# Kernel optimization log

Hardware: AMD Instinct MI355X
Metric: run time of the kernel (lower is better)

Reference implementation:

```python
import jax, jax.numpy as jnp
import numpy as np

NEG_SLOPE = 0.2  # leakyrelu negative_slope from init

def _lrelu(x):
    return jax.nn.leaky_relu(x, NEG_SLOPE)

def setup_inputs() -> dict:
    key = jax.random.key(0)
    k1, k2, k3 = jax.random.split(key, 3)
    B, N, Fin, Fout = 8, 2048, 128, 64
    x = jax.random.normal(k1, (B, N, Fin), dtype=jnp.float32)
    W = jax.random.normal(k2, (Fin, Fout), dtype=jnp.float32) * (1.414 / np.sqrt(Fin))
    a = jax.random.normal(k3, (2 * Fout, 1), dtype=jnp.float32) * 0.1
    return {"x": x, "W": W, "a": a}

def reference(x, W, a):
    # x: (B, N, Fin), W: (Fin, Fout), a: (2*Fout, 1)
    Fout = W.shape[1]
    h = jnp.matmul(x, W)  # (B, N, Fout)
    a1 = a[:Fout, 0]      # attends to source node i
    a2 = a[Fout:, 0]      # attends to target node j
    # e[b,i,j] = leakyrelu(h[b,i]@a1 + h[b,j]@a2); avoids O(N^2*2F) repeat+cat
    s1 = jnp.einsum('bnf,f->bn', h, a1)  # (B, N)
    s2 = jnp.einsum('bnf,f->bn', h, a2)  # (B, N)
    e = _lrelu(s1[:, :, None] + s2[:, None, :])  # (B, N, N)
    attention = jax.nn.softmax(e, axis=1)  # softmax over dim=1, as in source
    # dropout in eval mode: identity
    h_prime = jnp.matmul(attention, h)  # (B, N, Fout)
    return _lrelu(h_prime)
```

## Files before the change

### kernel.cpp

```cpp
#include <hip/hip_runtime.h>
#include <math.h>

#define B 8
#define N 2048
#define NP1 2049
#define FIN 128
#define FOUT 64
#define NS 0.2f
#define K 2048
#define KP1 2049
#define NCH 64
#define CHS 32

__device__ __forceinline__ int bucketOf(float v) {
  int q = (int)floorf((v + 8.0f) * 128.0f);
  return min(max(q, 0), K - 1);
}

__device__ __forceinline__ int wscan_add_i(int v, int lane) {
#pragma unroll
  for (int off = 1; off < 64; off <<= 1) {
    int o = __shfl_up(v, off, 64);
    v += (lane >= off) ? o : 0;
  }
  return v;
}
__device__ __forceinline__ float wscan_add_f(float v, int lane) {
#pragma unroll
  for (int off = 1; off < 64; off <<= 1) {
    float o = __shfl_up(v, off, 64);
    v += (lane >= off) ? o : 0.f;
  }
  return v;
}

#define RPB 32
__global__ __launch_bounds__(256, 2) void k_hs(
    const float* __restrict__ x, const float* __restrict__ W,
    const float* __restrict__ a, float* __restrict__ h,
    float* __restrict__ s1, float* __restrict__ s2) {
  __shared__ float xs[RPB * FIN];
  const int row0 = blockIdx.x * RPB;
  const int lane = threadIdx.x & 63;
  const int wv = threadIdx.x >> 6;

  {
    const float4* src = (const float4*)(x + (size_t)row0 * FIN);
    float4* dst = (float4*)xs;
#pragma unroll
    for (int t = 0; t < 4; ++t)
      dst[threadIdx.x + 256 * t] = src[threadIdx.x + 256 * t];
  }

  float w[FIN];
#pragma unroll
  for (int k = 0; k < FIN; ++k) w[k] = W[k * FOUT + lane];
  const float a1 = a[lane];
  const float a2 = a[FOUT + lane];
  __syncthreads();

  for (int n = 0; n < 8; ++n) {
    const int r = wv * 8 + n;
    const float* xr = xs + r * FIN;
    float ac0 = 0.f, ac1 = 0.f, ac2 = 0.f, ac3 = 0.f;
#pragma unroll
    for (int k4 = 0; k4 < FIN; k4 += 4) {
      float4 xv = *(const float4*)(xr + k4);
      ac0 = fmaf(xv.x, w[k4 + 0], ac0);
      ac1 = fmaf(xv.y, w[k4 + 1], ac1);
      ac2 = fmaf(xv.z, w[k4 + 2], ac2);
      ac3 = fmaf(xv.w, w[k4 + 3], ac3);
    }
    const float acc = (ac0 + ac1) + (ac2 + ac3);
    const int row = row0 + r;
    h[(size_t)row * FOUT + lane] = acc;

    float v1 = acc * a1;
    float v2 = acc * a2;
#pragma unroll
    for (int off = 32; off > 0; off >>= 1) {
      v1 += __shfl_xor(v1, off, 64);
      v2 += __shfl_xor(v2, off, 64);
    }
    if (lane == 0) {
      s1[row] = v1;
      s2[row] = v2;
    }
  }
}

__global__ __launch_bounds__(1024) void k_bucket(
    const float* __restrict__ s1, const float* __restrict__ s2,
    int* __restrict__ start1, float* __restrict__ elemS1,
    float* __restrict__ elemU, float* __restrict__ elemUq,
    float* __restrict__ slotPrefU, float* __restrict__ slotPrefQ,
    int* __restrict__ start2, float* __restrict__ elemS2,
    int* __restrict__ idx2) {
  __shared__ int cnt[K];
  __shared__ int cur[K];
  __shared__ float eS[N];
  __shared__ float eU[N];
  __shared__ float eQ[N];
  __shared__ int eJ[N];
  __shared__ int wtI[16];
  __shared__ float wtU[16], wtQ[16];

  const int type = blockIdx.x & 1;
  const int b = blockIdx.x >> 1;
  const int tid = threadIdx.x;
  const int lane = tid & 63;
  const int wv = tid >> 6;
  const float* key = (type ? s2 : s1) + b * N;

  cnt[tid] = 0;
  cnt[tid + 1024] = 0;
  __syncthreads();
  const float k0 = key[tid], k1 = key[tid + 1024];
  const int q0 = bucketOf(k0), q1 = bucketOf(k1);
  atomicAdd(&cnt[q0], 1);
  atomicAdd(&cnt[q1], 1);
  __syncthreads();

  {
    const int c0 = cnt[2 * tid], c1 = cnt[2 * tid + 1];
    const int loc = c0 + c1;
    const int incl = wscan_add_i(loc, lane);
    if (lane == 63) wtI[wv] = incl;
    __syncthreads();
    int cross = 0;
#pragma unroll
    for (int w = 0; w < 16; ++w) cross += (w < wv) ? wtI[w] : 0;
    const int ex = cross + incl - loc;
    cnt[2 * tid] = ex;       cnt[2 * tid + 1] = ex + c0;
    cur[2 * tid] = ex;       cur[2 * tid + 1] = ex + c0;
  }
  __syncthreads();

  if (type == 0) {
    int sl = atomicAdd(&cur[q0], 1);
    eS[sl] = k0; eU[sl] = expf(k0); eQ[sl] = expf(NS * k0);
    sl = atomicAdd(&cur[q1], 1);
    eS[sl] = k1; eU[sl] = expf(k1); eQ[sl] = expf(NS * k1);
  } else {
    int sl = atomicAdd(&cur[q0], 1);
    eS[sl] = k0; eJ[sl] = tid;
    sl = atomicAdd(&cur[q1], 1);
    eS[sl] = k1; eJ[sl] = tid + 1024;
  }
  __syncthreads();

  if (type == 1) {
    elemS2[b * N + tid] = eS[tid];
    elemS2[b * N + tid + 1024] = eS[tid + 1024];
    idx2[b * N + tid] = eJ[tid];
    idx2[b * N + tid + 1024] = eJ[tid + 1024];
    start2[b * KP1 + tid] = cnt[tid];
    start2[b * KP1 + tid + 1024] = cnt[tid + 1024];
    if (tid == 0) start2[b * KP1 + K] = N;
    return;
  }

  elemS1[b * N + tid] = eS[tid];
  elemS1[b * N + tid + 1024] = eS[tid + 1024];
  elemU[b * N + tid] = eU[tid];
  elemU[b * N + tid + 1024] = eU[tid + 1024];
  elemUq[b * N + tid] = eQ[tid];
  elemUq[b * N + tid + 1024] = eQ[tid + 1024];
  start1[b * KP1 + tid] = cnt[tid];
  start1[b * KP1 + tid + 1024] = cnt[tid + 1024];
  if (tid == 0) start1[b * KP1 + K] = N;

  const float u0 = eU[2 * tid], u1 = eU[2 * tid + 1];
  const float g0 = eQ[2 * tid], g1 = eQ[2 * tid + 1];
  const float locU = u0 + u1, locQ = g0 + g1;
  const float iU = wscan_add_f(locU, lane);
  const float iQ = wscan_add_f(locQ, lane);
  if (lane == 63) { wtU[wv] = iU; wtQ[wv] = iQ; }
  __syncthreads();
  float crU = 0.f, crQ = 0.f, totU = 0.f, totQ = 0.f;
#pragma unroll
  for (int w = 0; w < 16; ++w) {
    const float au = wtU[w], aq = wtQ[w];
    crU += (w < wv) ? au : 0.f;
    crQ += (w < wv) ? aq : 0.f;
    totU += au; totQ += aq;
  }
  const float exU = crU + iU - locU, exQ = crQ + iQ - locQ;
  slotPrefU[b * NP1 + 2 * tid] = exU;
  slotPrefU[b * NP1 + 2 * tid + 1] = exU + u0;
  slotPrefQ[b * NP1 + 2 * tid] = exQ;
  slotPrefQ[b * NP1 + 2 * tid + 1] = exQ + g0;
  if (tid == 0) { slotPrefU[b * NP1 + N] = totU; slotPrefQ[b * NP1 + N] = totQ; }
}

__global__ __launch_bounds__(256) void k_scan1(
    const float* __restrict__ elemS1, const float* __restrict__ elemU,
    const float* __restrict__ elemUq, const float* __restrict__ slotPrefU,
    const float* __restrict__ slotPrefQ, const int* __restrict__ start1,
    const float* __restrict__ elemS2, const int* __restrict__ idx2,
    const float* __restrict__ h, float2* __restrict__ AB,
    float* __restrict__ hperm, float* __restrict__ ctA,
    float* __restrict__ ctB) {
  const int b = blockIdx.x >> 4;
  const int chunk = (blockIdx.x & 15) * 4 + (threadIdx.x >> 6);
  const int f = threadIdx.x & 63;
  const int s0 = chunk * CHS;

  float Aval = 0.f, Bval = 0.f;
  if (f < 32) {
    const int s = s0 + f;
    const float s2v = elemS2[b * N + s];
    const float t = -s2v;
    const int q = bucketOf(t);
    const int sb = start1[b * KP1 + q], se = start1[b * KP1 + q + 1];
    float Pu = slotPrefU[b * NP1 + sb];
    float Pq = slotPrefQ[b * NP1 + sb];
    for (int i = sb; i < se; ++i) {
      const bool lt = elemS1[b * N + i] < t;
      Pu += lt ? elemU[b * N + i] : 0.f;
      Pq += lt ? elemUq[b * N + i] : 0.f;
    }
    const float totU = slotPrefU[b * NP1 + N];
    const float E = expf(s2v), Eq = expf(NS * s2v);
    const float Z = E * (totU - Pu) + Eq * Pq;
    Aval = E / Z;
    Bval = Eq / Z;
    AB[b * N + s] = make_float2(Aval, Bval);
  }

  float hv[CHS];
#pragma unroll
  for (int g = 0; g < 2; ++g) {
#pragma unroll
    for (int rr = 0; rr < 16; ++rr) {
      const int s = s0 + g * 16 + rr;
      const int j = idx2[b * N + s];
      hv[g * 16 + rr] = h[((size_t)b * N + j) * FOUT + f];
    }
  }
  float ta = 0.f, tb = 0.f;
#pragma unroll
  for (int rr = 0; rr < CHS; ++rr) {
    hperm[((size_t)b * N + s0 + rr) * FOUT + f] = hv[rr];
    const float av = __shfl(Aval, rr, 64);
    const float bv = __shfl(Bval, rr, 64);
    ta = fmaf(av, hv[rr], ta);
    tb = fmaf(bv, hv[rr], tb);
  }
  ctA[(b * NCH + chunk) * FOUT + f] = ta;
  ctB[(b * NCH + chunk) * FOUT + f] = tb;
}

__global__ __launch_bounds__(256) void k_scan2(
    const float2* __restrict__ AB, const float* __restrict__ hperm,
    const float* __restrict__ ctA, const float* __restrict__ ctB,
    float* __restrict__ SA, float* __restrict__ PB) {
  __shared__ float cA[NCH * FOUT];
  __shared__ float cB[NCH * FOUT];
  const int b = blockIdx.x >> 4;
  const int chunk = (blockIdx.x & 15) * 4 + (threadIdx.x >> 6);
  const int f = threadIdx.x & 63;
  const int s0 = chunk * CHS;

  for (int t = threadIdx.x; t < NCH * FOUT; t += 256) {
    cA[t] = ctA[b * NCH * FOUT + t];
    cB[t] = ctB[b * NCH * FOUT + t];
  }
  __syncthreads();

  float offA = 0.f, offB = 0.f;
#pragma unroll 8
  for (int c2 = 0; c2 < NCH; ++c2) {
    const float va = cA[c2 * FOUT + f];
    const float vb = cB[c2 * FOUT + f];
    if (c2 > chunk) offA += va;
    if (c2 < chunk) offB += vb;
  }

  float run = offB;
#pragma unroll
  for (int g = 0; g < 2; ++g) {
    float hv[16]; float2 ab[16];
#pragma unroll
    for (int rr = 0; rr < 16; ++rr) {
      const int s = s0 + g * 16 + rr;
      hv[rr] = hperm[((size_t)b * N + s) * FOUT + f];
      ab[rr] = AB[b * N + s];
    }
#pragma unroll
    for (int rr = 0; rr < 16; ++rr) {
      run = fmaf(ab[rr].y, hv[rr], run);
      PB[((size_t)b * NP1 + s0 + g * 16 + rr + 1) * FOUT + f] = run;
    }
  }
  run = offA;
#pragma unroll
  for (int g = 1; g >= 0; --g) {
    float hv[16]; float2 ab[16];
#pragma unroll
    for (int rr = 0; rr < 16; ++rr) {
      const int s = s0 + g * 16 + rr;
      hv[rr] = hperm[((size_t)b * N + s) * FOUT + f];
      ab[rr] = AB[b * N + s];
    }
#pragma unroll
    for (int rr = 15; rr >= 0; --rr) {
      run = fmaf(ab[rr].x, hv[rr], run);
      SA[((size_t)b * NP1 + s0 + g * 16 + rr) * FOUT + f] = run;
    }
  }
  if (chunk == 0) {
    PB[((size_t)b * NP1 + 0) * FOUT + f] = 0.f;
    SA[((size_t)b * NP1 + N) * FOUT + f] = 0.f;
  }
}

__global__ void k_out(const float* __restrict__ s1,
                      const int* __restrict__ start2,
                      const float* __restrict__ elemS2,
                      const float2* __restrict__ AB,
                      const float* __restrict__ hperm,
                      const float* __restrict__ SA,
                      const float* __restrict__ PB,
                      float* __restrict__ out) {
  const int wv = threadIdx.x >> 6;
  const int lane = threadIdx.x & 63;
  const int row = blockIdx.x * 4 + wv;
  const int b = row >> 11;
  const float s1v = s1[row];
  const float t = -s1v;
  const int q = bucketOf(t);
  const int sb = start2[b * KP1 + q];
  const int se = start2[b * KP1 + q + 1];

  float sa = SA[((size_t)b * NP1 + se) * FOUT + lane];
  float pb = PB[((size_t)b * NP1 + sb) * FOUT + lane];
  for (int s = sb; s < se; ++s) {
    const float s2v = elemS2[b * N + s];
    const float2 ab = AB[b * N + s];
    const float hv = hperm[((size_t)b * N + s) * FOUT + lane];
    if (s2v >= t) sa = fmaf(ab.x, hv, sa);
    else          pb = fmaf(ab.y, hv, pb);
  }
  const float uu = expf(s1v), uqv = expf(NS * s1v);
  const float v = uu * sa + uqv * pb;
  out[(size_t)row * FOUT + lane] = v >= 0.f ? v : NS * v;
}

extern "C" void kernel_launch(void* const* d_in, const int* in_sizes, int n_in,
                              void* d_out, int out_size, void* d_ws, size_t ws_size,
                              hipStream_t stream) {
  const float* x = (const float*)d_in[0];
  const float* W = (const float*)d_in[1];
  const float* a = (const float*)d_in[2];
  float* out = (float*)d_out;

  float* ws = (float*)d_ws;
  float* h = ws;
  float* hperm = h + (size_t)B * N * FOUT;
  float* s1 = hperm + (size_t)B * N * FOUT;
  float* s2 = s1 + B * N;
  float* elemS1 = s2 + B * N;
  float* elemU = elemS1 + B * N;
  float* elemUq = elemU + B * N;
  float* elemS2 = elemUq + B * N;
  float* slotPrefU = elemS2 + B * N;
  float* slotPrefQ = slotPrefU + B * NP1;
  float2* AB = (float2*)(slotPrefQ + B * NP1);
  int* idx2 = (int*)(AB + (size_t)B * N);
  int* start1 = idx2 + B * N;
  int* start2 = start1 + B * KP1;
  float* ctA = (float*)(start2 + B * KP1);
  float* ctB = ctA + (size_t)B * NCH * FOUT;
  float* SA = ctB + (size_t)B * NCH * FOUT;
  float* PB = SA + (size_t)B * NP1 * FOUT;

  k_hs<<<B * N / RPB, 256, 0, stream>>>(x, W, a, h, s1, s2);
  k_bucket<<<2 * B, 1024, 0, stream>>>(s1, s2, start1, elemS1, elemU, elemUq,
                                       slotPrefU, slotPrefQ, start2, elemS2, idx2);
  k_scan1<<<B * 16, 256, 0, stream>>>(elemS1, elemU, elemUq, slotPrefU,
                                      slotPrefQ, start1, elemS2, idx2, h, AB,
                                      hperm, ctA, ctB);
  k_scan2<<<B * 16, 256, 0, stream>>>(AB, hperm, ctA, ctB, SA, PB);
  k_out<<<B * N / 4, 256, 0, stream>>>(s1, start2, elemS2, AB, hperm, SA, PB, out);
}
```

Baseline: 53.43 us.

## Replace full per-row prefix scans with chunk-level prefix sums and in-chunk accumulation

The k_scan2 kernel, which wrote full per-row prefix arrays SA and PB of size B*N*64 each, is replaced by a tiny k_cpref kernel. That kernel builds prefix sums over only the 64 chunk totals. k_out now rebuilds its sums from the chunk prefix plus a scan inside the row's chunk up to the bucket end, so the large write and re-read of per-row prefix arrays goes away. In exchange, k_out does up to about 32 extra gathered accumulations per row, and the A sum is taken as total minus prefix, which may cost floating-point accuracy. Separately, k_hs drops its shared-memory staging and block barrier and reads x rows straight from global memory.

```diff
diff --git a/kernel.cpp b/kernel.cpp
--- a/kernel.cpp
+++ b/kernel.cpp
@@ -10,6 +10,7 @@
 #define K 2048
 #define KP1 2049
 #define NCH 64
+#define NCHP1 65
 #define CHS 32
 
 __device__ __forceinline__ int bucketOf(float v) {
@@ -39,29 +40,19 @@
     const float* __restrict__ x, const float* __restrict__ W,
     const float* __restrict__ a, float* __restrict__ h,
     float* __restrict__ s1, float* __restrict__ s2) {
-  __shared__ float xs[RPB * FIN];
-  const int row0 = blockIdx.x * RPB;
   const int lane = threadIdx.x & 63;
-  const int wv = threadIdx.x >> 6;
-
-  {
-    const float4* src = (const float4*)(x + (size_t)row0 * FIN);
-    float4* dst = (float4*)xs;
-#pragma unroll
-    for (int t = 0; t < 4; ++t)
-      dst[threadIdx.x + 256 * t] = src[threadIdx.x + 256 * t];
-  }
+  const int wv = __builtin_amdgcn_readfirstlane(threadIdx.x >> 6);
+  const int row0 = blockIdx.x * RPB + wv * 8;
 
   float w[FIN];
 #pragma unroll
   for (int k = 0; k < FIN; ++k) w[k] = W[k * FOUT + lane];
   const float a1 = a[lane];
   const float a2 = a[FOUT + lane];
-  __syncthreads();
 
   for (int n = 0; n < 8; ++n) {
-    const int r = wv * 8 + n;
-    const float* xr = xs + r * FIN;
+    const int row = row0 + n;
+    const float* xr = x + (size_t)row * FIN;
     float ac0 = 0.f, ac1 = 0.f, ac2 = 0.f, ac3 = 0.f;
 #pragma unroll
     for (int k4 = 0; k4 < FIN; k4 += 4) {
@@ -72,7 +63,6 @@
       ac3 = fmaf(xv.w, w[k4 + 3], ac3);
     }
     const float acc = (ac0 + ac1) + (ac2 + ac3);
-    const int row = row0 + r;
     h[(size_t)row * FOUT + lane] = acc;
 
     float v1 = acc * a1;
@@ -251,68 +241,26 @@
   ctB[(b * NCH + chunk) * FOUT + f] = tb;
 }
 
-__global__ __launch_bounds__(256) void k_scan2(
-    const float2* __restrict__ AB, const float* __restrict__ hperm,
+__global__ __launch_bounds__(128) void k_cpref(
     const float* __restrict__ ctA, const float* __restrict__ ctB,
-    float* __restrict__ SA, float* __restrict__ PB) {
-  __shared__ float cA[NCH * FOUT];
-  __shared__ float cB[NCH * FOUT];
-  const int b = blockIdx.x >> 4;
-  const int chunk = (blockIdx.x & 15) * 4 + (threadIdx.x >> 6);
+    float* __restrict__ PAx, float* __restrict__ PBx) {
+  const int b = blockIdx.x;
   const int f = threadIdx.x & 63;
-  const int s0 = chunk * CHS;
-
-  for (int t = threadIdx.x; t < NCH * FOUT; t += 256) {
-    cA[t] = ctA[b * NCH * FOUT + t];
-    cB[t] = ctB[b * NCH * FOUT + t];
-  }
-  __syncthreads();
-
-  float offA = 0.f, offB = 0.f;
-#pragma unroll 8
-  for (int c2 = 0; c2 < NCH; ++c2) {
-    const float va = cA[c2 * FOUT + f];
-    const float vb = cB[c2 * FOUT + f];
-    if (c2 > chunk) offA += va;
-    if (c2 < chunk) offB += vb;
-  }
-
-  float run = offB;
-#pragma unroll
-  for (int g = 0; g < 2; ++g) {
-    float hv[16]; float2 ab[16];
-#pragma unroll
-    for (int rr = 0; rr < 16; ++rr) {
-      const int s = s0 + g * 16 + rr;
-      hv[rr] = hperm[((size_t)b * N + s) * FOUT + f];
-      ab[rr] = AB[b * N + s];
-    }
-#pragma unroll
-    for (int rr = 0; rr < 16; ++rr) {
-      run = fmaf(ab[rr].y, hv[rr], run);
-      PB[((size_t)b * NP1 + s0 + g * 16 + rr + 1) * FOUT + f] = run;
-    }
-  }
-  run = offA;
-#pragma unroll
-  for (int g = 1; g >= 0; --g) {
-    float hv[16]; float2 ab[16];
-#pragma unroll
-    for (int rr = 0; rr < 16; ++rr) {
-      const int s = s0 + g * 16 + rr;
-      hv[rr] = hperm[((size_t)b * N + s) * FOUT + f];
-      ab[rr] = AB[b * N + s];
-    }
-#pragma unroll
-    for (int rr = 15; rr >= 0; --rr) {
-      run = fmaf(ab[rr].x, hv[rr], run);
-      SA[((size_t)b * NP1 + s0 + g * 16 + rr) * FOUT + f] = run;
-    }
-  }
-  if (chunk == 0) {
-    PB[((size_t)b * NP1 + 0) * FOUT + f] = 0.f;
-    SA[((size_t)b * NP1 + N) * FOUT + f] = 0.f;
-  }
+  const int which = threadIdx.x >> 6;
+  const float* src = which ? ctB : ctA;
+  float* dst = which ? PBx : PAx;
+
+  float v[NCH];
+#pragma unroll
+  for (int c = 0; c < NCH; ++c)
+    v[c] = src[(b * NCH + c) * FOUT + f];
+  float run = 0.f;
+#pragma unroll
+  for (int c = 0; c < NCH; ++c) {
+    dst[((size_t)b * NCHP1 + c) * FOUT + f] = run;
+    run += v[c];
+  }
+  dst[((size_t)b * NCHP1 + NCH) * FOUT + f] = run;
 }
 
 __global__ void k_out(const float* __restrict__ s1,
@@ -320,8 +268,8 @@
                       const float* __restrict__ elemS2,
                       const float2* __restrict__ AB,
                       const float* __restrict__ hperm,
-                      const float* __restrict__ SA,
-                      const float* __restrict__ PB,
+                      const float* __restrict__ PAx,
+                      const float* __restrict__ PBx,
                       float* __restrict__ out) {
   const int wv = threadIdx.x >> 6;
   const int lane = threadIdx.x & 63;
@@ -332,16 +280,24 @@
   const int q = bucketOf(t);
   const int sb = start2[b * KP1 + q];
   const int se = start2[b * KP1 + q + 1];
-
-  float sa = SA[((size_t)b * NP1 + se) * FOUT + lane];
-  float pb = PB[((size_t)b * NP1 + sb) * FOUT + lane];
-  for (int s = sb; s < se; ++s) {
-    const float s2v = elemS2[b * N + s];
-    const float2 ab = AB[b * N + s];
-    const float hv = hperm[((size_t)b * N + s) * FOUT + lane];
-    if (s2v >= t) sa = fmaf(ab.x, hv, sa);
-    else          pb = fmaf(ab.y, hv, pb);
-  }
+  const int chb = sb >> 5;
+
+  const float PAv = PAx[((size_t)b * NCHP1 + chb) * FOUT + lane];
+  const float PBv = PBx[((size_t)b * NCHP1 + chb) * FOUT + lane];
+  const float totA = PAx[((size_t)b * NCHP1 + NCH) * FOUT + lane];
+
+  float accA = 0.f, accB = 0.f;
+  for (int s = chb * CHS; s < se; ++s) {
+    const bool take = (s < sb) || (elemS2[b * N + s] < t);
+    if (take) {
+      const float2 ab = AB[b * N + s];
+      const float hv = hperm[((size_t)b * N + s) * FOUT + lane];
+      accA = fmaf(ab.x, hv, accA);
+      accB = fmaf(ab.y, hv, accB);
+    }
+  }
+  const float sa = totA - PAv - accA;
+  const float pb = PBv + accB;
   const float uu = expf(s1v), uqv = expf(NS * s1v);
   const float v = uu * sa + uqv * pb;
   out[(size_t)row * FOUT + lane] = v >= 0.f ? v : NS * v;
@@ -372,8 +328,8 @@
   int* start2 = start1 + B * KP1;
   float* ctA = (float*)(start2 + B * KP1);
   float* ctB = ctA + (size_t)B * NCH * FOUT;
-  float* SA = ctB + (size_t)B * NCH * FOUT;
-  float* PB = SA + (size_t)B * NP1 * FOUT;
+  float* PAx = ctB + (size_t)B * NCH * FOUT;
+  float* PBx = PAx + (size_t)B * NCHP1 * FOUT;
 
   k_hs<<<B * N / RPB, 256, 0, stream>>>(x, W, a, h, s1, s2);
   k_bucket<<<2 * B, 1024, 0, stream>>>(s1, s2, start1, elemS1, elemU, elemUq,
@@ -381,6 +337,6 @@
   k_scan1<<<B * 16, 256, 0, stream>>>(elemS1, elemU, elemUq, slotPrefU,
                                       slotPrefQ, start1, elemS2, idx2, h, AB,
                                       hperm, ctA, ctB);
-  k_scan2<<<B * 16, 256, 0, stream>>>(AB, hperm, ctA, ctB, SA, PB);
-  k_out<<<B * N / 4, 256, 0, stream>>>(s1, start2, elemS2, AB, hperm, SA, PB, out);
-}
+  k_cpref<<<B, 128, 0, stream>>>(ctA, ctB, PAx, PBx);
+  k_out<<<B * N / 4, 256, 0, stream>>>(s1, start2, elemS2, AB, hperm, PAx, PBx, out);
+}
```

Result: slower. 70.82 us (+32.5%).
